# Optimization experiments

Measured on AMD Instinct MI355X. Metric: run time of the kernel, lower is better.

Reference implementation:

```python
import jax, jax.numpy as jnp
import numpy as np
import math

VOCAB = 32000
DIM = 1024
TOKENS = 4096
PAD_IDX = 0
NBITS = 4
QN = -(2 ** (NBITS - 1))        # -8
QP = 2 ** (NBITS - 1) - 1       # 7


def setup_inputs() -> dict:
    key = jax.random.key(0)
    k_idx, k_w = jax.random.split(key)
    idx = jax.random.randint(k_idx, (TOKENS,), 0, VOCAB)
    # x is one-hot over the vocabulary, as implied by topk(x,1)[1] extracting the index
    x = jax.nn.one_hot(idx, VOCAB, dtype=jnp.float32)
    weight = jax.random.normal(k_w, (DIM, VOCAB), dtype=jnp.float32) * 0.02
    # LSQ init rule: alpha = 2 * mean|W| / sqrt(Qp)
    alpha = (2.0 * jnp.mean(jnp.abs(weight)) / math.sqrt(QP)).reshape(1)
    return {"x": x, "weight": weight, "alpha": alpha}


def reference(x, weight, alpha):
    # topk(x, 1)[1] on a one-hot input == argmax over vocab
    idx = jnp.argmax(x, axis=-1)                       # [T]
    mask = (idx == PAD_IDX)[:, None]                   # [T, 1]
    a = alpha[0]
    # LSQ fake-quantize the weight: round(clamp(w/alpha, Qn, Qp)) * alpha
    w_q = jnp.round(jnp.clip(weight / a, QN, QP)) * a  # [DIM, VOCAB]
    out = jnp.einsum('tv,dv->td', x, w_q)              # [T, DIM]
    return jnp.where(mask, 0.0, out)
```

## Files before the change

### kernel.cpp

```cpp
#include <hip/hip_runtime.h>


typedef float        v4f __attribute__((ext_vector_type(4)));
typedef unsigned int v4u __attribute__((ext_vector_type(4)));
typedef unsigned int u32;

constexpr int VOCAB  = 32000;
constexpr int DIM    = 1024;
constexpr int TOKENS = 4096;
constexpr int V4     = VOCAB / 4;
constexpr int WPT    = 8;
constexpr int WIN    = 64 * WPT;
constexpr int NWIN   = V4 / WIN;
constexpr int TAILB  = NWIN * WIN;
constexpr int TAILC  = (V4 - TAILB) / 64;

__device__ __forceinline__ int word_of(v4u c) {
    return c.x ? 0 : (c.y ? 1 : (c.z ? 2 : 3));
}
__device__ __forceinline__ u32 nz(v4u c) { return c.x | c.y | c.z | c.w; }

__global__ __launch_bounds__(64) void emb_lsq_kernel(
    const float* __restrict__ x,
    const float* __restrict__ w,
    const float* __restrict__ alpha,
    float* __restrict__ out)
{
    const int lane = threadIdx.x;
    const int t    = blockIdx.x;

    const v4u* xr = reinterpret_cast<const v4u*>(x + (size_t)t * VOCAB);
    int  cand = -1;
    bool done = false;

    v4u A[WPT], B[WPT];
    #pragma unroll
    for (int j = 0; j < WPT; ++j) A[j] = xr[lane + 64 * j];

    #pragma unroll
    for (int k = 0; k < NWIN; ++k) {
        if (k + 1 < NWIN) {
            #pragma unroll
            for (int j = 0; j < WPT; ++j)
                B[j] = xr[(k + 1) * WIN + lane + 64 * j];
        }
        u32 m = 0;
        #pragma unroll
        for (int j = 0; j < WPT; ++j) m |= nz(A[j]);
        if (__ballot(m != 0)) {
            if (m) {
                #pragma unroll
                for (int j = 0; j < WPT; ++j)
                    if (nz(A[j])) cand = 4 * (k * WIN + lane + 64 * j) + word_of(A[j]);
            }
            done = true;
            break;
        }
        #pragma unroll
        for (int j = 0; j < WPT; ++j) A[j] = B[j];
    }
    if (!done) {
        #pragma unroll
        for (int j = 0; j < TAILC; ++j) {
            const int c = TAILB + lane + 64 * j;
            v4u v = xr[c];
            if (nz(v)) cand = 4 * c + word_of(v);
        }
    }
    const unsigned long long msk = __ballot(cand >= 0);
    const int idx = msk ? __shfl(cand, (int)__ffsll(msk) - 1) : 0;

    v4f* orow = reinterpret_cast<v4f*>(out + (size_t)t * DIM);
    if (idx <= 0) {
        v4f z = 0.f;
        #pragma unroll
        for (int j = 0; j < 4; ++j) orow[lane + 64 * j] = z;
    } else {
        const float a = alpha[0];
        const size_t col = (size_t)idx;
        float wv[16];
        #pragma unroll
        for (int j = 0; j < 4; ++j) {
            const int d0 = 4 * lane + 256 * j;
            wv[4*j+0] = w[(size_t)(d0 + 0) * VOCAB + col];
            wv[4*j+1] = w[(size_t)(d0 + 1) * VOCAB + col];
            wv[4*j+2] = w[(size_t)(d0 + 2) * VOCAB + col];
            wv[4*j+3] = w[(size_t)(d0 + 3) * VOCAB + col];
        }
        #pragma unroll
        for (int j = 0; j < 4; ++j) {
            v4f q;
            q.x = rintf(fminf(fmaxf(wv[4*j+0] / a, -8.f), 7.f)) * a;
            q.y = rintf(fminf(fmaxf(wv[4*j+1] / a, -8.f), 7.f)) * a;
            q.z = rintf(fminf(fmaxf(wv[4*j+2] / a, -8.f), 7.f)) * a;
            q.w = rintf(fminf(fmaxf(wv[4*j+3] / a, -8.f), 7.f)) * a;
            orow[lane + 64 * j] = q;
        }
    }
}

extern "C" void kernel_launch(void* const* d_in, const int* in_sizes, int n_in,
                              void* d_out, int out_size, void* d_ws, size_t ws_size,
                              hipStream_t stream) {
    const float* x     = (const float*)d_in[0];
    const float* w     = (const float*)d_in[1];
    const float* alpha = (const float*)d_in[2];
    float* out         = (float*)d_out;

    emb_lsq_kernel<<<TOKENS, 64, 0, stream>>>(x, w, alpha, out);
}
```

Measured before the change: 729.1 us.

## Split into a grid-wide streaming one-hot scan kernel and a separate gather kernel

Index extraction moves out of the per-token, single-wave kernel with serial early exit into its own kernel. That kernel streams the whole one-hot matrix across a full grid with non-temporal 16-byte loads and writes each token's index to workspace. A second kernel reads the index and does the quantized column gather. The aim is to saturate HBM bandwidth instead of being latency-bound per token. The cost is giving up the early exit: all of x is read rather than about half, and an extra launch is added.

```diff
diff --git a/kernel.cpp b/kernel.cpp
--- a/kernel.cpp
+++ b/kernel.cpp
@@ -9,66 +9,55 @@
 constexpr int DIM    = 1024;
 constexpr int TOKENS = 4096;
 constexpr int V4     = VOCAB / 4;
-constexpr int WPT    = 8;
-constexpr int WIN    = 64 * WPT;
-constexpr int NWIN   = V4 / WIN;
-constexpr int TAILB  = NWIN * WIN;
-constexpr int TAILC  = (V4 - TAILB) / 64;
+constexpr u32 NCHUNK = (u32)TOKENS * V4;
+constexpr int SBLK   = 2560;
+constexpr int STHR   = 256;
+constexpr u32 STRIDE = (u32)SBLK * STHR;
+constexpr int KPT    = NCHUNK / STRIDE;
 
+__device__ __forceinline__ u32 nz(v4u c) { return c.x | c.y | c.z | c.w; }
 __device__ __forceinline__ int word_of(v4u c) {
     return c.x ? 0 : (c.y ? 1 : (c.z ? 2 : 3));
 }
-__device__ __forceinline__ u32 nz(v4u c) { return c.x | c.y | c.z | c.w; }
 
-__global__ __launch_bounds__(64) void emb_lsq_kernel(
-    const float* __restrict__ x,
+__global__ __launch_bounds__(STHR) void scan_all_kernel(
+    const float* __restrict__ x, int* __restrict__ idxs)
+{
+    const u32 gid = blockIdx.x * STHR + threadIdx.x;
+    const v4u* xp = reinterpret_cast<const v4u*>(x);
+
+    #pragma unroll
+    for (int k0 = 0; k0 < KPT; k0 += 5) {
+        v4u c0 = __builtin_nontemporal_load(&xp[gid + (u32)(k0 + 0) * STRIDE]);
+        v4u c1 = __builtin_nontemporal_load(&xp[gid + (u32)(k0 + 1) * STRIDE]);
+        v4u c2 = __builtin_nontemporal_load(&xp[gid + (u32)(k0 + 2) * STRIDE]);
+        v4u c3 = __builtin_nontemporal_load(&xp[gid + (u32)(k0 + 3) * STRIDE]);
+        v4u c4 = __builtin_nontemporal_load(&xp[gid + (u32)(k0 + 4) * STRIDE]);
+        u32 h0 = nz(c0), h1 = nz(c1), h2 = nz(c2), h3 = nz(c3), h4 = nz(c4);
+        if (h0 | h1 | h2 | h3 | h4) {
+            #pragma unroll
+            for (int j = 0; j < 5; ++j) {
+                v4u c = j == 0 ? c0 : j == 1 ? c1 : j == 2 ? c2 : j == 3 ? c3 : c4;
+                if (nz(c)) {
+                    const u32 flat = gid + (u32)(k0 + j) * STRIDE;
+                    const u32 t    = flat / (u32)V4;
+                    const u32 cir  = flat - t * (u32)V4;
+                    idxs[t] = 4 * (int)cir + word_of(c);
+                }
+            }
+        }
+    }
+}
+
+__global__ __launch_bounds__(64) void gather_kernel(
     const float* __restrict__ w,
     const float* __restrict__ alpha,
+    const int* __restrict__ idxs,
     float* __restrict__ out)
 {
+    const int t    = blockIdx.x;
     const int lane = threadIdx.x;
-    const int t    = blockIdx.x;
-
-    const v4u* xr = reinterpret_cast<const v4u*>(x + (size_t)t * VOCAB);
-    int  cand = -1;
-    bool done = false;
-
-    v4u A[WPT], B[WPT];
-    #pragma unroll
-    for (int j = 0; j < WPT; ++j) A[j] = xr[lane + 64 * j];
-
-    #pragma unroll
-    for (int k = 0; k < NWIN; ++k) {
-        if (k + 1 < NWIN) {
-            #pragma unroll
-            for (int j = 0; j < WPT; ++j)
-                B[j] = xr[(k + 1) * WIN + lane + 64 * j];
-        }
-        u32 m = 0;
-        #pragma unroll
-        for (int j = 0; j < WPT; ++j) m |= nz(A[j]);
-        if (__ballot(m != 0)) {
-            if (m) {
-                #pragma unroll
-                for (int j = 0; j < WPT; ++j)
-                    if (nz(A[j])) cand = 4 * (k * WIN + lane + 64 * j) + word_of(A[j]);
-            }
-            done = true;
-            break;
-        }
-        #pragma unroll
-        for (int j = 0; j < WPT; ++j) A[j] = B[j];
-    }
-    if (!done) {
-        #pragma unroll
-        for (int j = 0; j < TAILC; ++j) {
-            const int c = TAILB + lane + 64 * j;
-            v4u v = xr[c];
-            if (nz(v)) cand = 4 * c + word_of(v);
-        }
-    }
-    const unsigned long long msk = __ballot(cand >= 0);
-    const int idx = msk ? __shfl(cand, (int)__ffsll(msk) - 1) : 0;
+    const int idx  = idxs[t];
 
     v4f* orow = reinterpret_cast<v4f*>(out + (size_t)t * DIM);
     if (idx <= 0) {
@@ -106,6 +95,8 @@
     const float* w     = (const float*)d_in[1];
     const float* alpha = (const float*)d_in[2];
     float* out         = (float*)d_out;
+    int*   idxs        = (int*)d_ws;
 
-    emb_lsq_kernel<<<TOKENS, 64, 0, stream>>>(x, w, alpha, out);
+    scan_all_kernel<<<SBLK, STHR, 0, stream>>>(x, idxs);
+    gather_kernel<<<TOKENS, 64, 0, stream>>>(w, alpha, idxs, out);
 }
```

Measured after the change: 760.4 us. 1.04x slower.
